# Optimization experiments

Hardware: AMD Instinct MI355X
Metric: run time of the kernel (lower is better)

Reference implementation:

```python
import jax, jax.numpy as jnp
import numpy as np

H = 1024        # hidden_dim
MD = 2048       # memory_dim
L = 16384       # memory length == max_length
N = 8           # head_N
# sys.float_info.min underflows to 0.0 in float32, exactly as in the torch
# original (python float * float32 tensor). Kept for faithfulness.
TINY = jnp.float32(2.2250738585072014e-308)


def setup_inputs() -> dict:
    key = jax.random.key(0)
    ks = jax.random.split(key, 12)
    s_h = 1.0 / np.sqrt(H)
    s_m = 1.0 / np.sqrt(MD)
    s_o = 1.0 / np.sqrt(2 * H)
    return {
        "x": jax.random.normal(ks[0], (1, 1, H), jnp.float32),
        "memory": jax.random.normal(ks[1], (L, MD), jnp.float32),
        "Wq": jax.random.uniform(ks[2], (H, H), jnp.float32, -s_h, s_h),
        "bq": jax.random.uniform(ks[3], (H,), jnp.float32, -s_h, s_h),
        "Wk": jax.random.uniform(ks[4], (H, MD), jnp.float32, -s_m, s_m),
        "bk": jax.random.uniform(ks[5], (H,), jnp.float32, -s_m, s_m),
        "Wv": jax.random.uniform(ks[6], (H, MD), jnp.float32, -s_m, s_m),
        "bv": jax.random.uniform(ks[7], (H,), jnp.float32, -s_m, s_m),
        "Wo": jax.random.uniform(ks[8], (H, 2 * H), jnp.float32, -s_o, s_o),
        "bo": jax.random.uniform(ks[9], (H,), jnp.float32, -s_o, s_o),
    }


def reference(x, memory, Wq, bq, Wk, bk, Wv, bv, Wo, bo):
    d = H // N  # per-head dim
    # Q: (1,H) -> (1,d,N) -> (N,1,d), scaled by d**-0.5
    q = x.reshape(1, -1) @ Wq.T + bq
    Q = q.reshape(1, d, N).transpose(2, 0, 1) * (d ** -0.5)
    # K: (L,H) -> (L,d,N) -> (N,d,L)
    K = (memory @ Wk.T + bk).reshape(-1, d, N).transpose(2, 1, 0)
    QK = jnp.einsum('nod,ndl->nol', Q, K)  # (N,1,L)
    # pad mask: 1 where the memory row sums to zero, else 0 (as in torch nonzero-set)
    any_zero = memory.sum(axis=1)
    pad_mask = (any_zero == 0).astype(QK.dtype)[None, None, :]
    QK = QK + pad_mask * TINY
    attn = jax.nn.softmax(QK, axis=-1)
    # V: (L,H) -> (L,d,N) -> (N,L,d)
    V = (memory @ Wv.T + bv).reshape(-1, d, N).transpose(2, 0, 1)
    feat = jnp.einsum('nol,nld->nod', attn, V)      # (N,1,d)
    feat = feat.transpose(1, 2, 0).reshape(1, 1, H)  # (1,1,H)
    ax = jnp.concatenate([x, feat], axis=-1)         # (1,1,2H)
    return jax.nn.relu(ax @ Wo.T + bo)
```

## Files before the change

### kernel.cpp

```cpp
#include <hip/hip_runtime.h>
#include <math.h>

#define LROWS 16384
#define HDIM  1024
#define MDIM  2048
#define NH    8
#define RSQRT_D 0.08838834764831844f

#define OFF_W     0
#define OFF_BETA  16384
#define OFF_Z     16392
#define OFF_Q     16400
#define OFF_FEAT  17424
#define OFF_Y     18448
#define OFF_YBUF  34832

__device__ __forceinline__ float dot4(float4 a, float4 b) {
  return a.x * b.x + a.y * b.y + a.z * b.z + a.w * b.w;
}
__device__ __forceinline__ void fma4(float4& acc, float s, float4 v) {
  acc.x = fmaf(s, v.x, acc.x); acc.y = fmaf(s, v.y, acc.y);
  acc.z = fmaf(s, v.z, acc.z); acc.w = fmaf(s, v.w, acc.w);
}
__device__ __forceinline__ void add4(float4& a, float4 v) {
  a.x += v.x; a.y += v.y; a.z += v.z; a.w += v.w;
}

__global__ __launch_bounds__(256) void k1_q(const float* __restrict__ x,
                                            const float* __restrict__ Wq,
                                            const float* __restrict__ bq,
                                            const float* __restrict__ bk,
                                            float* __restrict__ ws) {
  int tid = threadIdx.x, lane = tid & 63;
  int j = blockIdx.x * 4 + (tid >> 6);
  const float4* xr = (const float4*)x;
  const float4* wr = (const float4*)(Wq + (size_t)j * HDIM);
  float acc = 0.f;
#pragma unroll
  for (int i = 0; i < 4; ++i) {
    int idx = i * 64 + lane;
    acc += dot4(xr[idx], wr[idx]);
  }
#pragma unroll
  for (int off = 32; off; off >>= 1) acc += __shfl_xor(acc, off);
  if (lane == 0) {
    float qj = acc + bq[j];
    ws[OFF_Q + j] = qj;
    atomicAdd(&ws[OFF_BETA + (j & 7)], qj * bk[j]);
  }
}

__global__ __launch_bounds__(256) void k2_w(const float* __restrict__ Wk,
                                            float* __restrict__ ws) {
  int tid = threadIdx.x;
  int mc = blockIdx.x & 7, cc = blockIdx.x >> 3;
  int m = mc * 256 + tid;
  const float* q = ws + OFF_Q;
  float acc[8];
#pragma unroll
  for (int n = 0; n < 8; ++n) acc[n] = 0.f;
  int c0 = cc * 64;
  for (int c = c0; c < c0 + 64; c += 8) {
#pragma unroll
    for (int u = 0; u < 8; ++u)
      acc[u] = fmaf(q[c + u], Wk[(size_t)(c + u) * MDIM + m], acc[u]);
  }
#pragma unroll
  for (int n = 0; n < 8; ++n) atomicAdd(&ws[OFF_W + n * MDIM + m], acc[n]);
}

__global__ __launch_bounds__(256, 2) void k35(const float* __restrict__ mem,
                                              float* __restrict__ ws) {
  __shared__ float sred[4 * 32 * 33];
  __shared__ float4 pv4[32];
  int tid = threadIdx.x, lane = tid & 63, wv = tid >> 6;
  const float* wmat = ws + OFF_W;
  float* pv = (float*)pv4;

  float4 y0[8], y1[8];
#pragma unroll
  for (int n = 0; n < 8; ++n) {
    y0[n] = make_float4(0.f, 0.f, 0.f, 0.f);
    y1[n] = make_float4(0.f, 0.f, 0.f, 0.f);
  }
  float zacc = 0.f;

  for (int g = 0; g < 2; ++g) {
    int r0 = blockIdx.x * 32 + g * 16;
    float acc[4][8];
#pragma unroll
    for (int rr = 0; rr < 4; ++rr)
#pragma unroll
      for (int n = 0; n < 8; ++n) acc[rr][n] = 0.f;
    for (int step = 0; step < 8; ++step) {
      int mq = step * 64 + lane;
      float4 wvv[8];
#pragma unroll
      for (int n = 0; n < 8; ++n)
        wvv[n] = *(const float4*)(wmat + n * MDIM + mq * 4);
#pragma unroll
      for (int rr = 0; rr < 4; ++rr) {
        float4 mv = *(const float4*)(mem + (size_t)(r0 + wv * 4 + rr) * MDIM + mq * 4);
#pragma unroll
        for (int n = 0; n < 8; ++n) {
          acc[rr][n] = fmaf(mv.x, wvv[n].x, acc[rr][n]);
          acc[rr][n] = fmaf(mv.y, wvv[n].y, acc[rr][n]);
          acc[rr][n] = fmaf(mv.z, wvv[n].z, acc[rr][n]);
          acc[rr][n] = fmaf(mv.w, wvv[n].w, acc[rr][n]);
        }
      }
    }
#pragma unroll
    for (int rr = 0; rr < 4; ++rr)
#pragma unroll
      for (int n = 0; n < 8; ++n) acc[rr][n] += __shfl_xor(acc[rr][n], 32);
    if (lane < 32) {
#pragma unroll
      for (int rr = 0; rr < 4; ++rr)
#pragma unroll
        for (int n = 0; n < 8; ++n)
          sred[wv * 1056 + lane * 33 + rr * 8 + n] = acc[rr][n];
    }
    __syncthreads();
    if (tid < 128) {
      int rowl = tid >> 3, n = tid & 7;
      int wvx = rowl >> 2, rr = rowl & 3;
      const float* base = sred + wvx * 1056 + rr * 8 + n;
      float s = 0.f;
#pragma unroll
      for (int l = 0; l < 32; ++l) s += base[l * 33];
      s = (s + ws[OFF_BETA + n]) * RSQRT_D;
      float p = __expf(s);
      pv[rowl * 8 + n] = p;
      zacc += p;
    }
    __syncthreads();
#pragma unroll 4
    for (int rl = 0; rl < 16; ++rl) {
      const float* row = mem + (size_t)(r0 + rl) * MDIM;
      float4 m0 = *(const float4*)(row + tid * 4);
      float4 m1 = *(const float4*)(row + 1024 + tid * 4);
      float4 pA = pv4[rl * 2];
      float4 pB = pv4[rl * 2 + 1];
      fma4(y0[0], pA.x, m0); fma4(y1[0], pA.x, m1);
      fma4(y0[1], pA.y, m0); fma4(y1[1], pA.y, m1);
      fma4(y0[2], pA.z, m0); fma4(y1[2], pA.z, m1);
      fma4(y0[3], pA.w, m0); fma4(y1[3], pA.w, m1);
      fma4(y0[4], pB.x, m0); fma4(y1[4], pB.x, m1);
      fma4(y0[5], pB.y, m0); fma4(y1[5], pB.y, m1);
      fma4(y0[6], pB.z, m0); fma4(y1[6], pB.z, m1);
      fma4(y0[7], pB.w, m0); fma4(y1[7], pB.w, m1);
    }
    __syncthreads();
  }
  float* yb = ws + OFF_YBUF + (size_t)blockIdx.x * 16384;
#pragma unroll
  for (int n = 0; n < 8; ++n) {
    *(float4*)(yb + n * MDIM + tid * 4) = y0[n];
    *(float4*)(yb + n * MDIM + 1024 + tid * 4) = y1[n];
  }
  if (tid < 128) {
    float z = zacc;
    z += __shfl_xor(z, 8); z += __shfl_xor(z, 16); z += __shfl_xor(z, 32);
    if ((tid & 63) < 8) atomicAdd(&ws[OFF_Z + (tid & 7)], z);
  }
}

__global__ __launch_bounds__(256) void k4c(float* __restrict__ ws) {
  __shared__ float4 sA[256];
  int t = threadIdx.x;
  int quad = blockIdx.x * 16 + (t & 15);
  int b0 = (t >> 4) * 32;
  const float4* src = (const float4*)(ws + OFF_YBUF);
  float4 acc = make_float4(0.f, 0.f, 0.f, 0.f);
  for (int b = b0; b < b0 + 32; ++b)
    add4(acc, src[(size_t)b * 4096 + quad]);
  sA[(t & 15) * 16 + (t >> 4)] = acc;
  __syncthreads();
  if (t < 16) {
    float4 s = sA[t * 16];
#pragma unroll
    for (int j = 1; j < 16; ++j) add4(s, sA[t * 16 + j]);
    ((float4*)(ws + OFF_Y))[blockIdx.x * 16 + t] = s;
  }
}

__global__ __launch_bounds__(256) void k6_feat(const float* __restrict__ Wv,
                                               const float* __restrict__ bv,
                                               float* __restrict__ ws) {
  int tid = threadIdx.x, lane = tid & 63;
  int c = blockIdx.x * 4 + (tid >> 6);
  int n = c & 7;
  const float4* yb = (const float4*)(ws + OFF_Y + n * MDIM);
  const float4* wb = (const float4*)(Wv + (size_t)c * MDIM);
  float acc = 0.f;
#pragma unroll
  for (int s = 0; s < 8; ++s) {
    int idx = s * 64 + lane;
    acc += dot4(yb[idx], wb[idx]);
  }
#pragma unroll
  for (int off = 32; off; off >>= 1) acc += __shfl_xor(acc, off);
  if (lane == 0) ws[OFF_FEAT + c] = acc / ws[OFF_Z + n] + bv[c];
}

__global__ __launch_bounds__(256) void k7_out(const float* __restrict__ x,
                                              const float* __restrict__ Wo,
                                              const float* __restrict__ bo,
                                              const float* __restrict__ ws,
                                              float* __restrict__ out) {
  int tid = threadIdx.x, lane = tid & 63;
  int j = blockIdx.x * 4 + (tid >> 6);
  const float4* wb = (const float4*)(Wo + (size_t)j * 2048);
  const float4* xr = (const float4*)x;
  const float4* fr = (const float4*)(ws + OFF_FEAT);
  float acc = 0.f;
#pragma unroll
  for (int s = 0; s < 4; ++s) {
    int idx = s * 64 + lane;
    acc += dot4(xr[idx], wb[idx]);
    acc += dot4(fr[idx], wb[256 + idx]);
  }
#pragma unroll
  for (int off = 32; off; off >>= 1) acc += __shfl_xor(acc, off);
  if (lane == 0) out[j] = fmaxf(acc + bo[j], 0.f);
}

extern "C" void kernel_launch(void* const* d_in, const int* in_sizes, int n_in,
                              void* d_out, int out_size, void* d_ws, size_t ws_size,
                              hipStream_t stream) {
  const float* x   = (const float*)d_in[0];
  const float* mem = (const float*)d_in[1];
  const float* Wq  = (const float*)d_in[2];
  const float* bq  = (const float*)d_in[3];
  const float* Wk  = (const float*)d_in[4];
  const float* bk  = (const float*)d_in[5];
  const float* Wv  = (const float*)d_in[6];
  const float* bv  = (const float*)d_in[7];
  const float* Wo  = (const float*)d_in[8];
  const float* bo  = (const float*)d_in[9];
  float* ws  = (float*)d_ws;
  float* out = (float*)d_out;

  hipMemsetAsync(ws, 0, OFF_Q * sizeof(float), stream);

  k1_q   <<<256, 256, 0, stream>>>(x, Wq, bq, bk, ws);
  k2_w   <<<128, 256, 0, stream>>>(Wk, ws);
  k35    <<<512, 256, 0, stream>>>(mem, ws);
  k4c    <<<256, 256, 0, stream>>>(ws);
  k6_feat<<<256, 256, 0, stream>>>(Wv, bv, ws);
  k7_out <<<256, 256, 0, stream>>>(x, Wo, bo, ws, out);
}
```

Before: 300.7 us.

## Restructure k35 score pass to 8 rows per wave with double-buffered loads

The k35 score phase now has each wave handle 8 memory rows in one pass instead of two 16-row groups, so the W vectors are loaded once per step for more rows. Memory loads are double-buffered in registers, in both the score phase and the weighted-sum phase, to overlap them with FMA work. The shared reduction layout changes to padded float4 stores, and one barrier per group is removed. k2_w uses twice as many blocks, each covering half the columns. The costs are much higher register pressure (acc[8][8] plus two buffers), which risks spilling or lower occupancy under launch_bounds(256,2), and more atomics in k2_w.

```diff
diff --git a/kernel.cpp b/kernel.cpp
--- a/kernel.cpp
+++ b/kernel.cpp
@@ -4,7 +4,6 @@
 #define LROWS 16384
 #define HDIM  1024
 #define MDIM  2048
-#define NH    8
 #define RSQRT_D 0.08838834764831844f
 
 #define OFF_W     0
@@ -59,8 +58,8 @@
   float acc[8];
 #pragma unroll
   for (int n = 0; n < 8; ++n) acc[n] = 0.f;
-  int c0 = cc * 64;
-  for (int c = c0; c < c0 + 64; c += 8) {
+  int c0 = cc * 32;
+  for (int c = c0; c < c0 + 32; c += 8) {
 #pragma unroll
     for (int u = 0; u < 8; ++u)
       acc[u] = fmaf(q[c + u], Wk[(size_t)(c + u) * MDIM + m], acc[u]);
@@ -71,11 +70,81 @@
 
 __global__ __launch_bounds__(256, 2) void k35(const float* __restrict__ mem,
                                               float* __restrict__ ws) {
-  __shared__ float sred[4 * 32 * 33];
-  __shared__ float4 pv4[32];
+  __shared__ float sred[4][32][68];
+  __shared__ float4 pv4[64];
   int tid = threadIdx.x, lane = tid & 63, wv = tid >> 6;
   const float* wmat = ws + OFF_W;
-  float* pv = (float*)pv4;
+  int r0 = blockIdx.x * 32;
+  int rw = r0 + wv * 8;
+
+  float acc[8][8];
+#pragma unroll
+  for (int rr = 0; rr < 8; ++rr)
+#pragma unroll
+    for (int n = 0; n < 8; ++n) acc[rr][n] = 0.f;
+
+  float4 wvv[8];
+  float4 mv[2][8];
+
+  auto loadW = [&](int s) {
+    int mq = s * 64 + lane;
+#pragma unroll
+    for (int n = 0; n < 8; ++n)
+      wvv[n] = *(const float4*)(wmat + n * MDIM + mq * 4);
+  };
+  auto loadM = [&](int s, int b) {
+    int mq = s * 64 + lane;
+#pragma unroll
+    for (int rr = 0; rr < 8; ++rr)
+      mv[b][rr] = *(const float4*)(mem + (size_t)(rw + rr) * MDIM + mq * 4);
+  };
+
+  loadM(0, 0);
+#pragma unroll
+  for (int s = 0; s < 8; ++s) {
+    int cur = s & 1;
+    loadW(s);
+    if (s < 7) loadM(s + 1, cur ^ 1);
+#pragma unroll
+    for (int rr = 0; rr < 8; ++rr) {
+      float4 m = mv[cur][rr];
+#pragma unroll
+      for (int n = 0; n < 8; ++n) {
+        acc[rr][n] = fmaf(m.x, wvv[n].x, acc[rr][n]);
+        acc[rr][n] = fmaf(m.y, wvv[n].y, acc[rr][n]);
+        acc[rr][n] = fmaf(m.z, wvv[n].z, acc[rr][n]);
+        acc[rr][n] = fmaf(m.w, wvv[n].w, acc[rr][n]);
+      }
+    }
+  }
+#pragma unroll
+  for (int rr = 0; rr < 8; ++rr)
+#pragma unroll
+    for (int n = 0; n < 8; ++n) acc[rr][n] += __shfl_xor(acc[rr][n], 32);
+  if (lane < 32) {
+#pragma unroll
+    for (int j = 0; j < 16; ++j) {
+      int rr = j >> 1, n0 = (j & 1) * 4;
+      *(float4*)&sred[wv][lane][j * 4] =
+          make_float4(acc[rr][n0], acc[rr][n0 + 1], acc[rr][n0 + 2], acc[rr][n0 + 3]);
+    }
+  }
+  __syncthreads();
+
+  {
+    int row = tid >> 3, n = tid & 7;
+    int wvs = row >> 3, v = (row & 7) * 8 + n;
+    float ssum = 0.f;
+#pragma unroll
+    for (int l = 0; l < 32; ++l) ssum += sred[wvs][l][v];
+    float sc = (ssum + ws[OFF_BETA + n]) * RSQRT_D;
+    float p = __expf(sc);
+    ((float*)pv4)[tid] = p;
+    float z = p;
+    z += __shfl_xor(z, 8); z += __shfl_xor(z, 16); z += __shfl_xor(z, 32);
+    if (lane < 8) atomicAdd(&ws[OFF_Z + lane], z);
+  }
+  __syncthreads();
 
   float4 y0[8], y1[8];
 #pragma unroll
@@ -83,65 +152,26 @@
     y0[n] = make_float4(0.f, 0.f, 0.f, 0.f);
     y1[n] = make_float4(0.f, 0.f, 0.f, 0.f);
   }
-  float zacc = 0.f;
-
-  for (int g = 0; g < 2; ++g) {
-    int r0 = blockIdx.x * 32 + g * 16;
-    float acc[4][8];
-#pragma unroll
-    for (int rr = 0; rr < 4; ++rr)
-#pragma unroll
-      for (int n = 0; n < 8; ++n) acc[rr][n] = 0.f;
-    for (int step = 0; step < 8; ++step) {
-      int mq = step * 64 + lane;
-      float4 wvv[8];
-#pragma unroll
-      for (int n = 0; n < 8; ++n)
-        wvv[n] = *(const float4*)(wmat + n * MDIM + mq * 4);
-#pragma unroll
-      for (int rr = 0; rr < 4; ++rr) {
-        float4 mv = *(const float4*)(mem + (size_t)(r0 + wv * 4 + rr) * MDIM + mq * 4);
-#pragma unroll
-        for (int n = 0; n < 8; ++n) {
-          acc[rr][n] = fmaf(mv.x, wvv[n].x, acc[rr][n]);
-          acc[rr][n] = fmaf(mv.y, wvv[n].y, acc[rr][n]);
-          acc[rr][n] = fmaf(mv.z, wvv[n].z, acc[rr][n]);
-          acc[rr][n] = fmaf(mv.w, wvv[n].w, acc[rr][n]);
-        }
-      }
-    }
-#pragma unroll
-    for (int rr = 0; rr < 4; ++rr)
-#pragma unroll
-      for (int n = 0; n < 8; ++n) acc[rr][n] += __shfl_xor(acc[rr][n], 32);
-    if (lane < 32) {
-#pragma unroll
-      for (int rr = 0; rr < 4; ++rr)
-#pragma unroll
-        for (int n = 0; n < 8; ++n)
-          sred[wv * 1056 + lane * 33 + rr * 8 + n] = acc[rr][n];
-    }
-    __syncthreads();
-    if (tid < 128) {
-      int rowl = tid >> 3, n = tid & 7;
-      int wvx = rowl >> 2, rr = rowl & 3;
-      const float* base = sred + wvx * 1056 + rr * 8 + n;
-      float s = 0.f;
-#pragma unroll
-      for (int l = 0; l < 32; ++l) s += base[l * 33];
-      s = (s + ws[OFF_BETA + n]) * RSQRT_D;
-      float p = __expf(s);
-      pv[rowl * 8 + n] = p;
-      zacc += p;
-    }
-    __syncthreads();
-#pragma unroll 4
-    for (int rl = 0; rl < 16; ++rl) {
-      const float* row = mem + (size_t)(r0 + rl) * MDIM;
-      float4 m0 = *(const float4*)(row + tid * 4);
-      float4 m1 = *(const float4*)(row + 1024 + tid * 4);
+  float4 mb[2][8];
+  auto loadB = [&](int i, int b) {
+#pragma unroll
+    for (int rr = 0; rr < 4; ++rr) {
+      const float* row = mem + (size_t)(r0 + i * 4 + rr) * MDIM;
+      mb[b][rr * 2]     = *(const float4*)(row + tid * 4);
+      mb[b][rr * 2 + 1] = *(const float4*)(row + 1024 + tid * 4);
+    }
+  };
+  loadB(0, 0);
+#pragma unroll
+  for (int i = 0; i < 8; ++i) {
+    int cur = i & 1;
+    if (i < 7) loadB(i + 1, cur ^ 1);
+#pragma unroll
+    for (int rr = 0; rr < 4; ++rr) {
+      int rl = i * 4 + rr;
       float4 pA = pv4[rl * 2];
       float4 pB = pv4[rl * 2 + 1];
+      float4 m0 = mb[cur][rr * 2], m1 = mb[cur][rr * 2 + 1];
       fma4(y0[0], pA.x, m0); fma4(y1[0], pA.x, m1);
       fma4(y0[1], pA.y, m0); fma4(y1[1], pA.y, m1);
       fma4(y0[2], pA.z, m0); fma4(y1[2], pA.z, m1);
@@ -151,18 +181,12 @@
       fma4(y0[6], pB.z, m0); fma4(y1[6], pB.z, m1);
       fma4(y0[7], pB.w, m0); fma4(y1[7], pB.w, m1);
     }
-    __syncthreads();
   }
   float* yb = ws + OFF_YBUF + (size_t)blockIdx.x * 16384;
 #pragma unroll
   for (int n = 0; n < 8; ++n) {
     *(float4*)(yb + n * MDIM + tid * 4) = y0[n];
     *(float4*)(yb + n * MDIM + 1024 + tid * 4) = y1[n];
-  }
-  if (tid < 128) {
-    float z = zacc;
-    z += __shfl_xor(z, 8); z += __shfl_xor(z, 16); z += __shfl_xor(z, 32);
-    if ((tid & 63) < 8) atomicAdd(&ws[OFF_Z + (tid & 7)], z);
   }
 }
 
@@ -245,7 +269,7 @@
   hipMemsetAsync(ws, 0, OFF_Q * sizeof(float), stream);
 
   k1_q   <<<256, 256, 0, stream>>>(x, Wq, bq, bk, ws);
-  k2_w   <<<128, 256, 0, stream>>>(Wk, ws);
+  k2_w   <<<256, 256, 0, stream>>>(Wk, ws);
   k35    <<<512, 256, 0, stream>>>(mem, ws);
   k4c    <<<256, 256, 0, stream>>>(ws);
   k6_feat<<<256, 256, 0, stream>>>(Wv, bv, ws);
```

After: 313.6 us. 4.3% more time.

## Restructure k35 so each thread keeps a fixed column slice with register W and prefetch

Applied to the files above, without the earlier changes.

The fused score/weighted-sum kernel now assigns each thread a fixed 8-float column slice of the memory row. The matching W slices stay in registers for all 32 rows, which replaces the earlier scheme of reloading W per step over 4-row groups. Each row's scores are reduced with a full wave shuffle and a small shared-memory sum, and memory rows are software-prefetched four rows ahead in both passes. The k2_w grid is also doubled with half the columns per block to add parallelism. The trade-off is more shuffle reduction work per row and higher register pressure from holding W, prefetch buffers and 16 accumulators.

```diff
diff --git a/kernel.cpp b/kernel.cpp
--- a/kernel.cpp
+++ b/kernel.cpp
@@ -4,7 +4,6 @@
 #define LROWS 16384
 #define HDIM  1024
 #define MDIM  2048
-#define NH    8
 #define RSQRT_D 0.08838834764831844f
 
 #define OFF_W     0
@@ -59,8 +58,8 @@
   float acc[8];
 #pragma unroll
   for (int n = 0; n < 8; ++n) acc[n] = 0.f;
-  int c0 = cc * 64;
-  for (int c = c0; c < c0 + 64; c += 8) {
+  int c0 = cc * 32;
+  for (int c = c0; c < c0 + 32; c += 8) {
 #pragma unroll
     for (int u = 0; u < 8; ++u)
       acc[u] = fmaf(q[c + u], Wk[(size_t)(c + u) * MDIM + m], acc[u]);
@@ -71,98 +70,108 @@
 
 __global__ __launch_bounds__(256, 2) void k35(const float* __restrict__ mem,
                                               float* __restrict__ ws) {
-  __shared__ float sred[4 * 32 * 33];
-  __shared__ float4 pv4[32];
+  __shared__ float sred[4][32][8];
+  __shared__ float4 pv4[64];
+  float* pvf = (float*)pv4;
   int tid = threadIdx.x, lane = tid & 63, wv = tid >> 6;
-  const float* wmat = ws + OFF_W;
-  float* pv = (float*)pv4;
-
-  float4 y0[8], y1[8];
+  int r0 = blockIdx.x * 32;
+  int q0 = wv * 128 + lane;
+  const float4* W4 = (const float4*)(ws + OFF_W);
+  const float4* M4 = (const float4*)mem;
+
+  float4 wr[8][2];
 #pragma unroll
   for (int n = 0; n < 8; ++n) {
-    y0[n] = make_float4(0.f, 0.f, 0.f, 0.f);
-    y1[n] = make_float4(0.f, 0.f, 0.f, 0.f);
-  }
-  float zacc = 0.f;
-
-  for (int g = 0; g < 2; ++g) {
-    int r0 = blockIdx.x * 32 + g * 16;
-    float acc[4][8];
-#pragma unroll
-    for (int rr = 0; rr < 4; ++rr)
-#pragma unroll
-      for (int n = 0; n < 8; ++n) acc[rr][n] = 0.f;
-    for (int step = 0; step < 8; ++step) {
-      int mq = step * 64 + lane;
-      float4 wvv[8];
-#pragma unroll
-      for (int n = 0; n < 8; ++n)
-        wvv[n] = *(const float4*)(wmat + n * MDIM + mq * 4);
-#pragma unroll
-      for (int rr = 0; rr < 4; ++rr) {
-        float4 mv = *(const float4*)(mem + (size_t)(r0 + wv * 4 + rr) * MDIM + mq * 4);
-#pragma unroll
-        for (int n = 0; n < 8; ++n) {
-          acc[rr][n] = fmaf(mv.x, wvv[n].x, acc[rr][n]);
-          acc[rr][n] = fmaf(mv.y, wvv[n].y, acc[rr][n]);
-          acc[rr][n] = fmaf(mv.z, wvv[n].z, acc[rr][n]);
-          acc[rr][n] = fmaf(mv.w, wvv[n].w, acc[rr][n]);
-        }
-      }
-    }
-#pragma unroll
-    for (int rr = 0; rr < 4; ++rr)
-#pragma unroll
-      for (int n = 0; n < 8; ++n) acc[rr][n] += __shfl_xor(acc[rr][n], 32);
-    if (lane < 32) {
-#pragma unroll
-      for (int rr = 0; rr < 4; ++rr)
-#pragma unroll
-        for (int n = 0; n < 8; ++n)
-          sred[wv * 1056 + lane * 33 + rr * 8 + n] = acc[rr][n];
-    }
-    __syncthreads();
-    if (tid < 128) {
-      int rowl = tid >> 3, n = tid & 7;
-      int wvx = rowl >> 2, rr = rowl & 3;
-      const float* base = sred + wvx * 1056 + rr * 8 + n;
-      float s = 0.f;
-#pragma unroll
-      for (int l = 0; l < 32; ++l) s += base[l * 33];
-      s = (s + ws[OFF_BETA + n]) * RSQRT_D;
-      float p = __expf(s);
-      pv[rowl * 8 + n] = p;
-      zacc += p;
-    }
-    __syncthreads();
+    wr[n][0] = W4[n * 512 + q0];
+    wr[n][1] = W4[n * 512 + q0 + 64];
+  }
+
+  float4 mv[4][2];
+#pragma unroll
+  for (int k = 0; k < 4; ++k) {
+    mv[k][0] = M4[(size_t)(r0 + k) * 512 + q0];
+    mv[k][1] = M4[(size_t)(r0 + k) * 512 + q0 + 64];
+  }
 #pragma unroll 4
-    for (int rl = 0; rl < 16; ++rl) {
-      const float* row = mem + (size_t)(r0 + rl) * MDIM;
-      float4 m0 = *(const float4*)(row + tid * 4);
-      float4 m1 = *(const float4*)(row + 1024 + tid * 4);
-      float4 pA = pv4[rl * 2];
-      float4 pB = pv4[rl * 2 + 1];
-      fma4(y0[0], pA.x, m0); fma4(y1[0], pA.x, m1);
-      fma4(y0[1], pA.y, m0); fma4(y1[1], pA.y, m1);
-      fma4(y0[2], pA.z, m0); fma4(y1[2], pA.z, m1);
-      fma4(y0[3], pA.w, m0); fma4(y1[3], pA.w, m1);
-      fma4(y0[4], pB.x, m0); fma4(y1[4], pB.x, m1);
-      fma4(y0[5], pB.y, m0); fma4(y1[5], pB.y, m1);
-      fma4(y0[6], pB.z, m0); fma4(y1[6], pB.z, m1);
-      fma4(y0[7], pB.w, m0); fma4(y1[7], pB.w, m1);
-    }
-    __syncthreads();
-  }
-  float* yb = ws + OFF_YBUF + (size_t)blockIdx.x * 16384;
+  for (int r = 0; r < 32; ++r) {
+    int b = r & 3;
+    float4 m0 = mv[b][0], m1 = mv[b][1];
+    if (r + 4 < 32) {
+      mv[b][0] = M4[(size_t)(r0 + r + 4) * 512 + q0];
+      mv[b][1] = M4[(size_t)(r0 + r + 4) * 512 + q0 + 64];
+    }
+    float a[8];
+#pragma unroll
+    for (int n = 0; n < 8; ++n) {
+      float t;
+      t = m0.x * wr[n][0].x;
+      t = fmaf(m0.y, wr[n][0].y, t);
+      t = fmaf(m0.z, wr[n][0].z, t);
+      t = fmaf(m0.w, wr[n][0].w, t);
+      t = fmaf(m1.x, wr[n][1].x, t);
+      t = fmaf(m1.y, wr[n][1].y, t);
+      t = fmaf(m1.z, wr[n][1].z, t);
+      t = fmaf(m1.w, wr[n][1].w, t);
+      a[n] = t;
+    }
+#pragma unroll
+    for (int mask = 1; mask <= 32; mask <<= 1)
+#pragma unroll
+      for (int n = 0; n < 8; ++n) a[n] += __shfl_xor(a[n], mask);
+    if (lane == 0) {
+      *(float4*)&sred[wv][r][0] = make_float4(a[0], a[1], a[2], a[3]);
+      *(float4*)&sred[wv][r][4] = make_float4(a[4], a[5], a[6], a[7]);
+    }
+  }
+  __syncthreads();
+
+  {
+    int row = tid >> 3, h = tid & 7;
+    float s = sred[0][row][h] + sred[1][row][h] + sred[2][row][h] + sred[3][row][h];
+    s = (s + ws[OFF_BETA + h]) * RSQRT_D;
+    float p = __expf(s);
+    pvf[tid] = p;
+    float z = p;
+    z += __shfl_xor(z, 8); z += __shfl_xor(z, 16); z += __shfl_xor(z, 32);
+    if (lane < 8) atomicAdd(&ws[OFF_Z + lane], z);
+  }
+  __syncthreads();
+
+  float4 y[8][2];
 #pragma unroll
   for (int n = 0; n < 8; ++n) {
-    *(float4*)(yb + n * MDIM + tid * 4) = y0[n];
-    *(float4*)(yb + n * MDIM + 1024 + tid * 4) = y1[n];
-  }
-  if (tid < 128) {
-    float z = zacc;
-    z += __shfl_xor(z, 8); z += __shfl_xor(z, 16); z += __shfl_xor(z, 32);
-    if ((tid & 63) < 8) atomicAdd(&ws[OFF_Z + (tid & 7)], z);
+    y[n][0] = make_float4(0.f, 0.f, 0.f, 0.f);
+    y[n][1] = make_float4(0.f, 0.f, 0.f, 0.f);
+  }
+#pragma unroll
+  for (int k = 0; k < 4; ++k) {
+    mv[k][0] = M4[(size_t)(r0 + k) * 512 + q0];
+    mv[k][1] = M4[(size_t)(r0 + k) * 512 + q0 + 64];
+  }
+#pragma unroll 4
+  for (int r = 0; r < 32; ++r) {
+    int b = r & 3;
+    float4 m0 = mv[b][0], m1 = mv[b][1];
+    if (r + 4 < 32) {
+      mv[b][0] = M4[(size_t)(r0 + r + 4) * 512 + q0];
+      mv[b][1] = M4[(size_t)(r0 + r + 4) * 512 + q0 + 64];
+    }
+    float4 pA = pv4[r * 2];
+    float4 pB = pv4[r * 2 + 1];
+    fma4(y[0][0], pA.x, m0); fma4(y[0][1], pA.x, m1);
+    fma4(y[1][0], pA.y, m0); fma4(y[1][1], pA.y, m1);
+    fma4(y[2][0], pA.z, m0); fma4(y[2][1], pA.z, m1);
+    fma4(y[3][0], pA.w, m0); fma4(y[3][1], pA.w, m1);
+    fma4(y[4][0], pB.x, m0); fma4(y[4][1], pB.x, m1);
+    fma4(y[5][0], pB.y, m0); fma4(y[5][1], pB.y, m1);
+    fma4(y[6][0], pB.z, m0); fma4(y[6][1], pB.z, m1);
+    fma4(y[7][0], pB.w, m0); fma4(y[7][1], pB.w, m1);
+  }
+  float4* YB4 = (float4*)(ws + OFF_YBUF + (size_t)blockIdx.x * 16384);
+#pragma unroll
+  for (int n = 0; n < 8; ++n) {
+    YB4[n * 512 + q0] = y[n][0];
+    YB4[n * 512 + q0 + 64] = y[n][1];
   }
 }
 
@@ -245,7 +254,7 @@
   hipMemsetAsync(ws, 0, OFF_Q * sizeof(float), stream);
 
   k1_q   <<<256, 256, 0, stream>>>(x, Wq, bq, bk, ws);
-  k2_w   <<<128, 256, 0, stream>>>(Wk, ws);
+  k2_w   <<<256, 256, 0, stream>>>(Wk, ws);
   k35    <<<512, 256, 0, stream>>>(mem, ws);
   k4c    <<<256, 256, 0, stream>>>(ws);
   k6_feat<<<256, 256, 0, stream>>>(Wv, bv, ws);
```

Measured after the change: 314.8 us. 4.7% more time.
